# Kernel tuning notes

Hardware: AMD Instinct MI355X
Metric: run time of the kernel (lower is better)

Reference implementation:

```python
import jax, jax.numpy as jnp
import numpy as np

N = 4096  # out_features (rows of W)
M = 4096  # in_features (cols of W)
S = 2048  # number of Givens pairs per side (= N//2)
TOKENS = 2048
EPS = 1e-8


def setup_inputs() -> dict:
    key = jax.random.key(0)
    ks = jax.random.split(key, 6)
    x = jax.random.normal(ks[0], (TOKENS, M), dtype=jnp.float32)
    W = jax.random.normal(ks[1], (N, M), dtype=jnp.float32) * (1.0 / np.sqrt(M))
    bias = jax.random.normal(ks[2], (N,), dtype=jnp.float32) * 0.02
    theta_L = 0.02 * jax.random.normal(ks[3], (S,), dtype=jnp.float32)
    theta_R = 0.02 * jax.random.normal(ks[4], (S,), dtype=jnp.float32)
    ecd_log_mag = jnp.zeros((N,), dtype=jnp.float32)
    # disjoint index pairs: (0,1),(2,3),... as produced by a permutation reshape
    pairs_L = jnp.arange(N, dtype=jnp.int64).reshape(S, 2)
    pairs_R = jnp.arange(M, dtype=jnp.int64).reshape(S, 2)
    return {"x": x, "W": W, "bias": bias, "theta_L": theta_L,
            "theta_R": theta_R, "ecd_log_mag": ecd_log_mag,
            "pairs_L": pairs_L, "pairs_R": pairs_R}


def _apply_left_rotations(W, theta, pairs):
    # Plane (Givens) rotations on disjoint row pairs of W: [S] angles, [S,2] indices
    c = jnp.cos(theta)[:, None]
    s = jnp.sin(theta)[:, None]
    i, j = pairs[:, 0], pairs[:, 1]
    ri, rj = W[i], W[j]                       # [S, M] gathers
    return W.at[i].set(c * ri - s * rj).at[j].set(s * ri + c * rj)


def _apply_right_rotations(W, theta, pairs):
    # Plane rotations on disjoint column pairs of W
    c = jnp.cos(theta)
    s = jnp.sin(theta)
    p, q = pairs[:, 0], pairs[:, 1]
    cp, cq = W[:, p], W[:, q]                 # [N, S] gathers
    return W.at[:, p].set(c * cp - s * cq).at[:, q].set(s * cp + c * cq)


def reference(x, W, bias, theta_L, theta_R, ecd_log_mag, pairs_L, pairs_R):
    # base row norms are buffers computed under no_grad from the frozen base weight
    base_row_norms = jax.lax.stop_gradient(jnp.linalg.norm(W, axis=1))  # [N]
    Wp = _apply_left_rotations(W, theta_L, pairs_L)
    Wp = _apply_right_rotations(Wp, theta_R, pairs_R)
    # magnitude rescale: row-normalize rotated weight, scale by learned magnitude
    row_norm = jnp.linalg.norm(Wp, axis=1, keepdims=True)               # [N,1]
    mag = base_row_norms * jnp.exp(ecd_log_mag)                         # [N]
    W_eff = Wp * (mag[:, None] / (row_norm + EPS))                      # [N,M]
    return x @ W_eff.T + bias                                           # [T,N]
```

## Files before the change

### kernel.cpp

```cpp
#include <hip/hip_runtime.h>
#include <hip/hip_bf16.h>


#define GK 4096
#define GN 4096
#define GT 2048
#define NPAIR 2048

typedef __bf16 bf16x8 __attribute__((ext_vector_type(8)));
typedef float  f32x4  __attribute__((ext_vector_type(4)));

static __device__ __forceinline__ unsigned short f2bf(float f) {
    union { float f; unsigned int u; } v; v.f = f;
    unsigned int r = v.u + 0x7fffu + ((v.u >> 16) & 1u);
    return (unsigned short)(r >> 16);
}
static __device__ __forceinline__ unsigned int pack2bf(float a, float b) {
    return (unsigned int)f2bf(a) | ((unsigned int)f2bf(b) << 16);
}

__global__ __launch_bounds__(256) void sincos_pre(
    const float* __restrict__ thR, float2* __restrict__ csR)
{
    const int i = blockIdx.x * 256 + threadIdx.x;
    if (i < NPAIR) {
        const float t = thR[i];
        csR[i] = make_float2(cosf(t), sinf(t));
    }
}

__global__ __launch_bounds__(256) void prelude(
    const float* __restrict__ W, const float* __restrict__ thL,
    const float2* __restrict__ csR, const float* __restrict__ ecd,
    const float* __restrict__ x,
    unsigned short* __restrict__ Weff, unsigned short* __restrict__ Xbf)
{
    const int tid = threadIdx.x;

    if (blockIdx.x >= 2048) {
        const int cb = blockIdx.x - 2048;
        const size_t base = (size_t)cb * 512;
        const float4* X4 = (const float4*)x;
        uint4* O4 = (uint4*)Xbf;
#pragma unroll
        for (int k = 0; k < 2; k++) {
            const size_t m = base + tid + k * 256;
            const float4 a = X4[2 * m];
            const float4 b = X4[2 * m + 1];
            uint4 o;
            o.x = pack2bf(a.x, a.y);
            o.y = pack2bf(a.z, a.w);
            o.z = pack2bf(b.x, b.y);
            o.w = pack2bf(b.z, b.w);
            O4[m] = o;
        }
        return;
    }

    const int s  = blockIdx.x;
    const int i0 = 2 * s, i1 = 2 * s + 1;

    const float tl = thL[s];
    const float cL = cosf(tl), sL = sinf(tl);

    float4 b0[4], b1[4];
    float s00 = 0.f, s11 = 0.f, s01 = 0.f;

    const float4* r0  = (const float4*)(W + (size_t)i0 * GK);
    const float4* r1  = (const float4*)(W + (size_t)i1 * GK);
    const float4* CS4 = (const float4*)csR;

#pragma unroll
    for (int k = 0; k < 4; k++) {
        const int c4 = tid + k * 256;
        const float4 w0 = r0[c4];
        const float4 w1 = r1[c4];
        const float4 cs = CS4[c4];
        s00 += w0.x * w0.x + w0.y * w0.y + w0.z * w0.z + w0.w * w0.w;
        s11 += w1.x * w1.x + w1.y * w1.y + w1.z * w1.z + w1.w * w1.w;
        s01 += w0.x * w1.x + w0.y * w1.y + w0.z * w1.z + w0.w * w1.w;
        const float a0x = cL * w0.x - sL * w1.x;
        const float a0y = cL * w0.y - sL * w1.y;
        const float a0z = cL * w0.z - sL * w1.z;
        const float a0w = cL * w0.w - sL * w1.w;
        const float a1x = sL * w0.x + cL * w1.x;
        const float a1y = sL * w0.y + cL * w1.y;
        const float a1z = sL * w0.z + cL * w1.z;
        const float a1w = sL * w0.w + cL * w1.w;
        b0[k].x = cs.x * a0x - cs.y * a0y;
        b0[k].y = cs.y * a0x + cs.x * a0y;
        b0[k].z = cs.z * a0z - cs.w * a0w;
        b0[k].w = cs.w * a0z + cs.z * a0w;
        b1[k].x = cs.x * a1x - cs.y * a1y;
        b1[k].y = cs.y * a1x + cs.x * a1y;
        b1[k].z = cs.z * a1z - cs.w * a1w;
        b1[k].w = cs.w * a1z + cs.z * a1w;
    }

#pragma unroll
    for (int off = 32; off; off >>= 1) {
        s00 += __shfl_down(s00, off);
        s11 += __shfl_down(s11, off);
        s01 += __shfl_down(s01, off);
    }
    __shared__ float red[3][4];
    __shared__ float scales[2];
    const int wave = tid >> 6, lane = tid & 63;
    if (lane == 0) { red[0][wave] = s00; red[1][wave] = s11; red[2][wave] = s01; }
    __syncthreads();
    if (tid == 0) {
        const float t0 = red[0][0] + red[0][1] + red[0][2] + red[0][3];
        const float t1 = red[1][0] + red[1][1] + red[1][2] + red[1][3];
        const float td = red[2][0] + red[2][1] + red[2][2] + red[2][3];
        const float n0 = cL * cL * t0 + sL * sL * t1 - 2.f * cL * sL * td;
        const float n1 = sL * sL * t0 + cL * cL * t1 + 2.f * cL * sL * td;
        scales[0] = sqrtf(t0) * expf(ecd[i0]) / (sqrtf(n0) + 1e-8f);
        scales[1] = sqrtf(t1) * expf(ecd[i1]) / (sqrtf(n1) + 1e-8f);
    }
    __syncthreads();
    const float sc0 = scales[0], sc1 = scales[1];

    uint2* o0 = (uint2*)(Weff + (size_t)i0 * GK);
    uint2* o1 = (uint2*)(Weff + (size_t)i1 * GK);
#pragma unroll
    for (int k = 0; k < 4; k++) {
        const int c4 = tid + k * 256;
        uint2 p0, p1;
        p0.x = pack2bf(b0[k].x * sc0, b0[k].y * sc0);
        p0.y = pack2bf(b0[k].z * sc0, b0[k].w * sc0);
        p1.x = pack2bf(b1[k].x * sc1, b1[k].y * sc1);
        p1.y = pack2bf(b1[k].z * sc1, b1[k].w * sc1);
        o0[c4] = p0;
        o1[c4] = p1;
    }
}

static __device__ __forceinline__ void glds16(const unsigned short* g, unsigned short* l) {
    __builtin_amdgcn_global_load_lds(
        (const __attribute__((address_space(1))) unsigned int*)g,
        (__attribute__((address_space(3))) unsigned int*)l, 16, 0, 0);
}

__global__ __launch_bounds__(256, 2) void gemm_bt(
    const unsigned short* __restrict__ A,
    const unsigned short* __restrict__ B,
    const float* __restrict__ bias,
    float* __restrict__ C)
{
    constexpr int BM = 128, BN = 128, BK = 64;
    constexpr int NT = GK / BK;
    __shared__ unsigned short smem[2][2][BM * BK];

    const int tid  = threadIdx.x;
    const int lane = tid & 63;
    const int wave = tid >> 6;
    const int quad = lane >> 4;
    const int l16  = lane & 15;
    const int wm   = wave >> 1;
    const int wn   = wave & 1;
    const int bm   = blockIdx.y * BM;
    const int bn   = blockIdx.x * BN;

    const int lrow = lane >> 3;
    const int jlog = (lane & 7) ^ lrow;
    const unsigned short* gA[4];
    const unsigned short* gB[4];
    int loff[4];
#pragma unroll
    for (int j = 0; j < 4; j++) {
        const int chunk = j * 4 + wave;
        gA[j] = A + (size_t)(bm + chunk * 8 + lrow) * GK + jlog * 8;
        gB[j] = B + (size_t)(bn + chunk * 8 + lrow) * GK + jlog * 8;
        loff[j] = chunk * 512 + lane * 8;
    }

#define STAGE(buf, k0) do {                                               \
    _Pragma("unroll")                                                     \
    for (int j = 0; j < 4; j++) {                                         \
        glds16(gA[j] + (k0), &smem[buf][0][loff[j]]);                     \
        glds16(gB[j] + (k0), &smem[buf][1][loff[j]]);                     \
    } } while (0)

    f32x4 acc[4][4] = {};

#define COMPUTE(b) do {                                                   \
    const unsigned short* As_ = &smem[b][0][0];                           \
    const unsigned short* Bs_ = &smem[b][1][0];                           \
    bf16x8 aF[2][4], bF[2][4];                                            \
    _Pragma("unroll")                                                     \
    for (int kk = 0; kk < 2; kk++) {                                      \
        _Pragma("unroll")                                                 \
        for (int i = 0; i < 4; i++) {                                     \
            const int ps = ((quad + 4 * kk) ^ (l16 & 7)) * 8;             \
            aF[kk][i] = *(const bf16x8*)(As_ + (wm * 64 + i * 16 + l16) * BK + ps); \
            bF[kk][i] = *(const bf16x8*)(Bs_ + (wn * 64 + i * 16 + l16) * BK + ps); \
        } }                                                               \
    _Pragma("unroll")                                                     \
    for (int i = 0; i < 4; i++) {                                         \
        _Pragma("unroll")                                                 \
        for (int j = 0; j < 4; j++) {                                     \
            acc[i][j] = __builtin_amdgcn_mfma_f32_16x16x32_bf16(          \
                aF[0][i], bF[0][j], acc[i][j], 0, 0, 0);                  \
            acc[i][j] = __builtin_amdgcn_mfma_f32_16x16x32_bf16(          \
                aF[1][i], bF[1][j], acc[i][j], 0, 0, 0);                  \
        } }                                                               \
    } while (0)

    STAGE(0, 0);
    int cur = 0;
    for (int t = 0; t < NT - 1; ++t) {
        STAGE(cur ^ 1, (t + 1) * BK);
        __builtin_amdgcn_sched_barrier(0);
        asm volatile("s_waitcnt vmcnt(8)" ::: "memory");
        __builtin_amdgcn_s_barrier();
        __builtin_amdgcn_sched_barrier(0);
        COMPUTE(cur);
        __builtin_amdgcn_sched_barrier(0);
        __builtin_amdgcn_s_barrier();
        cur ^= 1;
    }
    asm volatile("s_waitcnt vmcnt(0)" ::: "memory");
    __builtin_amdgcn_s_barrier();
    __builtin_amdgcn_sched_barrier(0);
    COMPUTE(cur);

#undef STAGE
#undef COMPUTE

#pragma unroll
    for (int i = 0; i < 4; i++) {
        const int m = bm + wm * 64 + i * 16 + quad * 4;
#pragma unroll
        for (int j = 0; j < 4; j++) {
            const int n = bn + wn * 64 + j * 16 + l16;
            const float bv = bias[n];
#pragma unroll
            for (int r = 0; r < 4; r++)
                C[(size_t)(m + r) * GN + n] = acc[i][j][r] + bv;
        }
    }
}

extern "C" void kernel_launch(void* const* d_in, const int* in_sizes, int n_in,
                              void* d_out, int out_size, void* d_ws, size_t ws_size,
                              hipStream_t stream) {
    const float* x    = (const float*)d_in[0];
    const float* W    = (const float*)d_in[1];
    const float* bias = (const float*)d_in[2];
    const float* thL  = (const float*)d_in[3];
    const float* thR  = (const float*)d_in[4];
    const float* ecd  = (const float*)d_in[5];

    unsigned short* Weff = (unsigned short*)d_ws;
    unsigned short* Xbf  = (unsigned short*)((char*)d_ws + (size_t)GN * GK * 2);
    float2* csR = (float2*)((char*)d_ws + (size_t)GN * GK * 2 + (size_t)GT * GK * 2);

    float* out = (float*)d_out;

    sincos_pre<<<dim3(NPAIR / 256), dim3(256), 0, stream>>>(thR, csR);
    prelude<<<dim3(4096), dim3(256), 0, stream>>>(W, thL, csR, ecd, x, Weff, Xbf);
    gemm_bt<<<dim3(GN / 128, GT / 128), dim3(256), 0, stream>>>(Xbf, Weff, bias, out);
}
```

Before: 210.6 us.

## Widen GEMM tile to 128x256 with 8 waves, split-phase loads and block swizzle

The bf16 GEMM now uses 512-thread blocks covering a 128x256 output tile, so each block reuses its A tile across twice as many columns. The grid is remapped with a swizzle to group blocks for better L2 locality. Each K step is split into two half-steps, with global-to-LDS loads interleaved between them and MFMA phases run at raised wave priority. This cuts grid size to 256 blocks (about one per CU), which raises the risk of tail and occupancy effects and adds more barriers per iteration.

```diff
diff --git a/kernel.cpp b/kernel.cpp
--- a/kernel.cpp
+++ b/kernel.cpp
@@ -141,91 +141,136 @@
         (__attribute__((address_space(3))) unsigned int*)l, 16, 0, 0);
 }
 
-__global__ __launch_bounds__(256, 2) void gemm_bt(
+__global__ __launch_bounds__(512, 2) void gemm_bt(
     const unsigned short* __restrict__ A,
     const unsigned short* __restrict__ B,
     const float* __restrict__ bias,
     float* __restrict__ C)
 {
-    constexpr int BM = 128, BN = 128, BK = 64;
+    constexpr int BM = 128, BN = 256, BK = 64;
     constexpr int NT = GK / BK;
-    __shared__ unsigned short smem[2][2][BM * BK];
+    __shared__ unsigned short As[2][BM * BK];
+    __shared__ unsigned short Bs[2][BN * BK];
 
     const int tid  = threadIdx.x;
     const int lane = tid & 63;
     const int wave = tid >> 6;
     const int quad = lane >> 4;
     const int l16  = lane & 15;
-    const int wm   = wave >> 1;
-    const int wn   = wave & 1;
-    const int bm   = blockIdx.y * BM;
-    const int bn   = blockIdx.x * BN;
+    const int wm   = wave >> 2;
+    const int wn   = wave & 3;
+
+    const int flat = blockIdx.y * 16 + blockIdx.x;
+    const int swz  = (flat & 7) * 32 + (flat >> 3);
+    const int bn   = (swz >> 4) * BN;
+    const int bm   = (swz & 15) * BM;
 
     const int lrow = lane >> 3;
     const int jlog = (lane & 7) ^ lrow;
-    const unsigned short* gA[4];
+    const unsigned short* gA[2];
     const unsigned short* gB[4];
-    int loff[4];
+    int lA[2], lB[4];
+#pragma unroll
+    for (int j = 0; j < 2; j++) {
+        const int c = 2 * wave + j;
+        gA[j] = A + (size_t)(bm + c * 8 + lrow) * GK + jlog * 8;
+        lA[j] = c * 512 + lane * 8;
+    }
 #pragma unroll
     for (int j = 0; j < 4; j++) {
-        const int chunk = j * 4 + wave;
-        gA[j] = A + (size_t)(bm + chunk * 8 + lrow) * GK + jlog * 8;
-        gB[j] = B + (size_t)(bn + chunk * 8 + lrow) * GK + jlog * 8;
-        loff[j] = chunk * 512 + lane * 8;
-    }
-
-#define STAGE(buf, k0) do {                                               \
-    _Pragma("unroll")                                                     \
-    for (int j = 0; j < 4; j++) {                                         \
-        glds16(gA[j] + (k0), &smem[buf][0][loff[j]]);                     \
-        glds16(gB[j] + (k0), &smem[buf][1][loff[j]]);                     \
-    } } while (0)
+        const int c = 4 * wave + j;
+        gB[j] = B + (size_t)(bn + c * 8 + lrow) * GK + jlog * 8;
+        lB[j] = c * 512 + lane * 8;
+    }
+
+#define LOADF(buf, kk, aF, bF) do {                                           \
+    const int ps = (((kk) * 4 + quad) ^ (l16 & 7)) * 8;                       \
+    _Pragma("unroll")                                                         \
+    for (int i = 0; i < 4; i++)                                               \
+        aF[i] = *(const bf16x8*)&As[buf][(wm * 64 + i * 16 + l16) * BK + ps]; \
+    _Pragma("unroll")                                                         \
+    for (int j = 0; j < 4; j++)                                               \
+        bF[j] = *(const bf16x8*)&Bs[buf][(wn * 64 + j * 16 + l16) * BK + ps]; \
+} while (0)
+
+#define MFMA16(aF, bF) do {                                                   \
+    _Pragma("unroll")                                                         \
+    for (int i = 0; i < 4; i++)                                               \
+        _Pragma("unroll")                                                     \
+        for (int j = 0; j < 4; j++)                                           \
+            acc[i][j] = __builtin_amdgcn_mfma_f32_16x16x32_bf16(              \
+                aF[i], bF[j], acc[i][j], 0, 0, 0);                            \
+} while (0)
 
     f32x4 acc[4][4] = {};
 
-#define COMPUTE(b) do {                                                   \
-    const unsigned short* As_ = &smem[b][0][0];                           \
-    const unsigned short* Bs_ = &smem[b][1][0];                           \
-    bf16x8 aF[2][4], bF[2][4];                                            \
-    _Pragma("unroll")                                                     \
-    for (int kk = 0; kk < 2; kk++) {                                      \
-        _Pragma("unroll")                                                 \
-        for (int i = 0; i < 4; i++) {                                     \
-            const int ps = ((quad + 4 * kk) ^ (l16 & 7)) * 8;             \
-            aF[kk][i] = *(const bf16x8*)(As_ + (wm * 64 + i * 16 + l16) * BK + ps); \
-            bF[kk][i] = *(const bf16x8*)(Bs_ + (wn * 64 + i * 16 + l16) * BK + ps); \
-        } }                                                               \
-    _Pragma("unroll")                                                     \
-    for (int i = 0; i < 4; i++) {                                         \
-        _Pragma("unroll")                                                 \
-        for (int j = 0; j < 4; j++) {                                     \
-            acc[i][j] = __builtin_amdgcn_mfma_f32_16x16x32_bf16(          \
-                aF[0][i], bF[0][j], acc[i][j], 0, 0, 0);                  \
-            acc[i][j] = __builtin_amdgcn_mfma_f32_16x16x32_bf16(          \
-                aF[1][i], bF[1][j], acc[i][j], 0, 0, 0);                  \
-        } }                                                               \
-    } while (0)
-
-    STAGE(0, 0);
+    glds16(gA[0], &As[0][lA[0]]);
+    glds16(gA[1], &As[0][lA[1]]);
+    glds16(gB[0], &Bs[0][lB[0]]);
+    glds16(gB[1], &Bs[0][lB[1]]);
+    glds16(gB[2], &Bs[0][lB[2]]);
+    glds16(gB[3], &Bs[0][lB[3]]);
+
     int cur = 0;
     for (int t = 0; t < NT - 1; ++t) {
-        STAGE(cur ^ 1, (t + 1) * BK);
-        __builtin_amdgcn_sched_barrier(0);
-        asm volatile("s_waitcnt vmcnt(8)" ::: "memory");
+        const int k1  = (t + 1) * BK;
+        const int nxt = cur ^ 1;
+        glds16(gA[0] + k1, &As[nxt][lA[0]]);
+        glds16(gA[1] + k1, &As[nxt][lA[1]]);
+        glds16(gB[0] + k1, &Bs[nxt][lB[0]]);
+        __builtin_amdgcn_sched_barrier(0);
+        asm volatile("s_waitcnt vmcnt(3)" ::: "memory");
         __builtin_amdgcn_s_barrier();
         __builtin_amdgcn_sched_barrier(0);
-        COMPUTE(cur);
+        {
+            bf16x8 aF[4], bF[4];
+            LOADF(cur, 0, aF, bF);
+            asm volatile("s_waitcnt lgkmcnt(0)" ::: "memory");
+            __builtin_amdgcn_sched_barrier(0);
+            __builtin_amdgcn_s_setprio(1);
+            MFMA16(aF, bF);
+            __builtin_amdgcn_s_setprio(0);
+        }
         __builtin_amdgcn_sched_barrier(0);
         __builtin_amdgcn_s_barrier();
-        cur ^= 1;
+        __builtin_amdgcn_sched_barrier(0);
+        glds16(gB[1] + k1, &Bs[nxt][lB[1]]);
+        glds16(gB[2] + k1, &Bs[nxt][lB[2]]);
+        glds16(gB[3] + k1, &Bs[nxt][lB[3]]);
+        __builtin_amdgcn_sched_barrier(0);
+        {
+            bf16x8 aF[4], bF[4];
+            LOADF(cur, 1, aF, bF);
+            asm volatile("s_waitcnt lgkmcnt(0)" ::: "memory");
+            __builtin_amdgcn_sched_barrier(0);
+            __builtin_amdgcn_s_barrier();
+            __builtin_amdgcn_sched_barrier(0);
+            __builtin_amdgcn_s_setprio(1);
+            MFMA16(aF, bF);
+            __builtin_amdgcn_s_setprio(0);
+        }
+        cur = nxt;
     }
     asm volatile("s_waitcnt vmcnt(0)" ::: "memory");
     __builtin_amdgcn_s_barrier();
     __builtin_amdgcn_sched_barrier(0);
-    COMPUTE(cur);
-
-#undef STAGE
-#undef COMPUTE
+    {
+        bf16x8 aF[4], bF[4];
+        LOADF(cur, 0, aF, bF);
+        asm volatile("s_waitcnt lgkmcnt(0)" ::: "memory");
+        __builtin_amdgcn_sched_barrier(0);
+        MFMA16(aF, bF);
+    }
+    {
+        bf16x8 aF[4], bF[4];
+        LOADF(cur, 1, aF, bF);
+        asm volatile("s_waitcnt lgkmcnt(0)" ::: "memory");
+        __builtin_amdgcn_sched_barrier(0);
+        MFMA16(aF, bF);
+    }
+
+#undef LOADF
+#undef MFMA16
 
 #pragma unroll
     for (int i = 0; i < 4; i++) {
@@ -259,5 +304,5 @@
 
     sincos_pre<<<dim3(NPAIR / 256), dim3(256), 0, stream>>>(thR, csR);
     prelude<<<dim3(4096), dim3(256), 0, stream>>>(W, thL, csR, ecd, x, Weff, Xbf);
-    gemm_bt<<<dim3(GN / 128, GT / 128), dim3(256), 0, stream>>>(Xbf, Weff, bias, out);
-}
+    gemm_bt<<<dim3(16, 16), dim3(512), 0, stream>>>(Xbf, Weff, bias, out);
+}
```

Result: slower. 244.2 us (+16.0%).
